# Optimization experiments

Measured on AMD Instinct MI355X. Metric: run time of the kernel, lower is better.

The kernel has to match this reference:

```python
import jax, jax.numpy as jnp
from jax import lax
import numpy as np

G, K = 8, 9  # deformable groups, 3x3 kernel taps


def conv1x1_bn_relu(x, W, scale, bias):
    # Conv2d 1x1 (no bias) + folded eval-mode BatchNorm (per-channel scale/bias) + ReLU
    y = jnp.einsum('bchw,oc->bohw', x, W)
    return jax.nn.relu(y * scale[None, :, None, None] + bias[None, :, None, None])


def dcn_v2(feat, offset_feat, W_om, b_om, W_dcn, b_dcn):
    # Modulated deformable conv v2, 3x3, stride 1, pad 1, dilation 1,
    # deformable_groups=G, extra_offset_mask: offsets/mask predicted from offset_feat.
    B, C, H, W_ = feat.shape
    Cg = C // G
    om = lax.conv_general_dilated(offset_feat, W_om, (1, 1), ((1, 1), (1, 1)))
    om = om + b_om[None, :, None, None]              # [B, 3*G*K, H, W]
    o1, o2, m = jnp.split(om, 3, axis=1)
    off_y = o1.reshape(B, G, K, H, W_)
    off_x = o2.reshape(B, G, K, H, W_)
    mask = jax.nn.sigmoid(m).reshape(B, G, K, H, W_)
    dk = jnp.arange(3) - 1
    dkh = jnp.repeat(dk, 3)   # tap row offset,  k = kh*3 + kw
    dkw = jnp.tile(dk, 3)     # tap col offset
    hh = jnp.arange(H, dtype=feat.dtype)
    ww = jnp.arange(W_, dtype=feat.dtype)
    py = hh[None, None, None, :, None] + dkh[None, None, :, None, None].astype(feat.dtype) + off_y
    px = ww[None, None, None, None, :] + dkw[None, None, :, None, None].astype(feat.dtype) + off_x
    y0 = jnp.floor(py); x0 = jnp.floor(px)
    ty = py - y0; tx = px - x0
    xg = feat.reshape(B, G, Cg, H * W_)

    def gather(idx):  # idx [B,G,K,H,W] int32 -> [B,G,Cg,K,H,W]
        f = lambda xf, i: xf[:, i]
        return jax.vmap(jax.vmap(f))(xg, idx)

    val = jnp.zeros((B, G, Cg, K, H, W_), dtype=feat.dtype)
    y0i = y0.astype(jnp.int32); x0i = x0.astype(jnp.int32)
    for dy, wy in ((0, 1.0 - ty), (1, ty)):
        iy = y0i + dy
        vy = (iy >= 0) & (iy < H)
        iyc = jnp.clip(iy, 0, H - 1)
        for dx, wx in ((0, 1.0 - tx), (1, tx)):
            ix = x0i + dx
            v = vy & (ix >= 0) & (ix < W_)
            idx = iyc * W_ + jnp.clip(ix, 0, W_ - 1)
            w = (wy * wx) * v.astype(feat.dtype)      # zero-padding outside
            val = val + w[:, :, None] * gather(idx)
    val = val * mask[:, :, None]                      # modulation
    Wd = W_dcn.reshape(W_dcn.shape[0], G, Cg, K)      # [Cout, G, Cg, K]
    out = jnp.einsum('bgckhw,ogck->bohw', val, Wd) + b_dcn[None, :, None, None]
    return out


def setup_inputs() -> dict:
    key = jax.random.key(0)
    ks = jax.random.split(key, 16)
    B, C, H, W_ = 8, 128, 64, 64
    Cd = C // 2  # dcn out channels = 64
    d = {}
    d['feat_l'] = jax.random.normal(ks[0], (B, C, H, W_), jnp.float32)
    d['feat_s'] = jax.random.normal(ks[1], (B, C, H // 2, W_ // 2), jnp.float32)
    d['W_fsm'] = jax.random.normal(ks[2], (C, C), jnp.float32) / np.sqrt(C)
    d['s_fsm'] = 1.0 + 0.1 * jax.random.normal(ks[3], (C,), jnp.float32)
    d['b_fsm'] = 0.1 * jax.random.normal(ks[4], (C,), jnp.float32)
    d['W_off'] = jax.random.normal(ks[5], (C, 2 * C), jnp.float32) / np.sqrt(2 * C)
    d['s_off'] = 1.0 + 0.1 * jax.random.normal(ks[6], (C,), jnp.float32)
    d['b_off'] = 0.1 * jax.random.normal(ks[7], (C,), jnp.float32)
    d['W_om'] = 0.05 * jax.random.normal(ks[8], (3 * G * K, C, 3, 3), jnp.float32)
    d['b_om'] = jnp.zeros((3 * G * K,), jnp.float32)
    d['W_dcn'] = jax.random.normal(ks[9], (Cd, C, 3, 3), jnp.float32) / np.sqrt(C * 9)
    d['b_dcn'] = 0.1 * jax.random.normal(ks[10], (Cd,), jnp.float32)
    d['W_cat'] = jax.random.normal(ks[11], (C, Cd), jnp.float32) / np.sqrt(Cd)
    d['s_cat'] = 1.0 + 0.1 * jax.random.normal(ks[12], (C,), jnp.float32)
    d['b_cat'] = 0.1 * jax.random.normal(ks[13], (C,), jnp.float32)
    return d


def reference(feat_l, feat_s, W_fsm, s_fsm, b_fsm, W_off, s_off, b_off,
              W_om, b_om, W_dcn, b_dcn, W_cat, s_cat, b_cat):
    # nearest upsample x2 (F.interpolate nearest to feat_l spatial size)
    feat_up = jnp.repeat(jnp.repeat(feat_s, 2, axis=2), 2, axis=3)
    feat_arm = conv1x1_bn_relu(feat_l, W_fsm, s_fsm, b_fsm)
    offset = conv1x1_bn_relu(jnp.concatenate([feat_arm, feat_up * 2.0], axis=1),
                             W_off, s_off, b_off)
    feat_align = jax.nn.relu(dcn_v2(feat_up, offset, W_om, b_om, W_dcn, b_dcn))
    feat = conv1x1_bn_relu(feat_align, W_cat, s_cat, b_cat) + feat_arm
    return (feat, feat_arm)
```

## Files before the change

### kernel.cpp

```cpp
#include <hip/hip_runtime.h>


typedef __attribute__((ext_vector_type(8))) short short8;
typedef __attribute__((ext_vector_type(4))) float f32x4;
typedef _Float16 __attribute__((ext_vector_type(2))) h2;

static __device__ __forceinline__ unsigned short f2bf(float x) {
    union { float f; unsigned int u; } v; v.f = x;
    return (unsigned short)((v.u + 0x7FFF + ((v.u >> 16) & 1)) >> 16);
}
static __device__ __forceinline__ unsigned short f2h(float x) {
    union { _Float16 h; unsigned short u; } v; v.h = (_Float16)x;
    return v.u;
}

__global__ __launch_bounds__(256) void k_prepfs(const float* __restrict__ fs,
        uint4* __restrict__ fsT4, uint4* __restrict__ fsH4) {
    __shared__ unsigned short st[64 * 136];
    unsigned int* st32 = (unsigned int*)st;
    const int t = threadIdx.x;
    const int b = blockIdx.x >> 4;
    const int p0 = (blockIdx.x & 15) << 6;
    for (int i = t; i < 64 * 64; i += 256) {
        int c2 = i >> 6, px = i & 63;
        float v0 = fs[(((b << 7) + 2 * c2) << 10) + p0 + px];
        float v1 = fs[(((b << 7) + 2 * c2 + 1) << 10) + p0 + px];
        st32[px * 68 + c2] = (unsigned int)f2bf(v0) | ((unsigned int)f2bf(v1) << 16);
    }
    __syncthreads();
    for (int i = t; i < 64 * 16; i += 256) {
        int px = i >> 4, q = i & 15;
        fsT4[(((b << 10) + p0 + px) << 4) + q] = ((const uint4*)(st + px * 136))[q];
    }
    __syncthreads();
    for (int i = t; i < 64 * 64; i += 256) {
        int c2 = i >> 6, px = i & 63;
        float v0 = fs[(((b << 7) + 2 * c2) << 10) + p0 + px];
        float v1 = fs[(((b << 7) + 2 * c2 + 1) << 10) + p0 + px];
        st32[px * 68 + c2] = (unsigned int)f2h(v0) | ((unsigned int)f2h(v1) << 16);
    }
    __syncthreads();
    for (int i = t; i < 64 * 16; i += 256) {
        int px = i >> 4, q = i & 15;
        fsH4[(((b << 10) + p0 + px) << 4) + q] = ((const uint4*)(st + px * 136))[q];
    }
}

__global__ __launch_bounds__(256) void k_packall(
        const float* __restrict__ W_fsm, const float* __restrict__ W_off,
        const float* __restrict__ W_cat, const float* __restrict__ W_dcn,
        const float* __restrict__ W_om,
        unsigned short* __restrict__ wbfsm, unsigned short* __restrict__ wboff,
        unsigned short* __restrict__ wbcat, unsigned short* __restrict__ wbdcn,
        unsigned short* __restrict__ wb2) {
    int idx = blockIdx.x * 256 + threadIdx.x;
    int lane = idx & 63;
    int ml = lane & 15, kl = (lane >> 4) * 8;
    unsigned short tmp[8];
    if (idx < 2048) {
        int r = idx >> 6;
        int o = (r % 8) * 16 + ml, k0 = (r / 8) * 32 + kl;
#pragma unroll
        for (int j = 0; j < 8; j++) tmp[j] = f2bf(W_fsm[o * 128 + k0 + j]);
        ((uint4*)wbfsm)[idx] = *(const uint4*)tmp;
    } else if (idx < 6144) {
        int i2 = idx - 2048;
        int r = i2 >> 6;
        int o = (r % 8) * 16 + ml, k0 = (r / 8) * 32 + kl;
#pragma unroll
        for (int j = 0; j < 8; j++) {
            int k = k0 + j;
            float f = W_off[o * 256 + k];
            if (k >= 128) f *= 2.0f;
            tmp[j] = f2bf(f);
        }
        ((uint4*)wboff)[i2] = *(const uint4*)tmp;
    } else if (idx < 7168) {
        int i2 = idx - 6144;
        int r = i2 >> 6;
        int o = (r % 8) * 16 + ml, k0 = (r / 8) * 32 + kl;
#pragma unroll
        for (int j = 0; j < 8; j++) tmp[j] = f2bf(W_cat[o * 64 + k0 + j]);
        ((uint4*)wbcat)[i2] = *(const uint4*)tmp;
    } else if (idx < 16384) {
        int i2 = idx - 7168;
        int r = i2 >> 6;
        int o = (r & 3) * 16 + ml, k0 = (r >> 2) * 32 + kl;
#pragma unroll
        for (int j = 0; j < 8; j++) {
            int k = k0 + j;
            int g = k / 144;
            int rem = k - g * 144;
            tmp[j] = f2h(W_dcn[(o * 128 + g * 16 + (rem & 15)) * 9 + (rem >> 4)]);
        }
        ((uint4*)wbdcn)[i2] = *(const uint4*)tmp;
    } else if (idx < 53248) {
        int i2 = idx - 16384;
        int r = i2 >> 6;
        int nt = r & 15, kk = r >> 4;
        int tap = kk >> 2, cc = kk & 3;
        int o = nt * 16 + ml;
        int c0 = cc * 32 + kl;
#pragma unroll
        for (int j = 0; j < 8; j++) {
            float v = (o < 216) ? W_om[(o * 128 + (c0 + j)) * 9 + tap] : 0.0f;
            tmp[j] = f2bf(v);
        }
        ((uint4*)wb2)[i2] = *(const uint4*)tmp;
    }
}

__global__ __launch_bounds__(512, 4) void k12(const float* __restrict__ feat_l,
        const uint4* __restrict__ fsT4,
        const unsigned short* __restrict__ wbf, const unsigned short* __restrict__ wbo,
        const float* __restrict__ s_fsm, const float* __restrict__ b_fsm,
        const float* __restrict__ s_off, const float* __restrict__ b_off,
        float* __restrict__ feat_arm, unsigned short* __restrict__ offT) {
    __shared__ unsigned short A1[64 * 136];
    __shared__ unsigned short A2[64 * 264];
    float* E32 = (float*)A1;
    const int t = threadIdx.x;
    const int b = blockIdx.x >> 6;
    const int h = blockIdx.x & 63;
    const int hw0 = h << 6;
    unsigned int* A1w = (unsigned int*)A1;
    for (int i = t; i < 64 * 64; i += 512) {
        int c2 = i >> 6, px = i & 63;
        float v0 = feat_l[(((b << 7) + 2 * c2) << 12) + hw0 + px];
        float v1 = feat_l[(((b << 7) + 2 * c2 + 1) << 12) + hw0 + px];
        A1w[px * 68 + c2] = (unsigned int)f2bf(v0) | ((unsigned int)f2bf(v1) << 16);
    }
    {
        const int h2 = h >> 1;
        int px2 = t >> 4, q = t & 15;
        uint4 v = fsT4[(((b << 10) + (h2 << 5) + px2) << 4) + q];
        ((uint4*)(A2 + (2 * px2) * 264 + 128))[q] = v;
        ((uint4*)(A2 + (2 * px2 + 1) * 264 + 128))[q] = v;
    }
    __syncthreads();
    const int lane = t & 63;
    const int w = __builtin_amdgcn_readfirstlane(t >> 6);
    const int pq = w & 3;
    const int nh = w >> 2;
    const int m = lane & 15, ko = lane >> 4;
    f32x4 acc[4];
#pragma unroll
    for (int nt2 = 0; nt2 < 4; nt2++) acc[nt2] = (f32x4){0.f, 0.f, 0.f, 0.f};
#pragma unroll
    for (int kk = 0; kk < 4; kk++) {
        short8 av = *(const short8*)(A1 + (pq * 16 + m) * 136 + kk * 32 + ko * 8);
        const uint4* wb = (const uint4*)wbf + (kk * 8 + nh * 4) * 64 + lane;
#pragma unroll
        for (int nt2 = 0; nt2 < 4; nt2++) {
            uint4 bu = wb[nt2 * 64];
            acc[nt2] = __builtin_amdgcn_mfma_f32_16x16x32_bf16(av, *(short8*)&bu, acc[nt2], 0, 0, 0);
        }
    }
#pragma unroll
    for (int nt2 = 0; nt2 < 4; nt2++) {
        int o = ((nh << 2) + nt2) * 16 + m;
        float sc = s_fsm[o], bi = b_fsm[o];
#pragma unroll
        for (int r = 0; r < 4; r++) {
            float v = fmaf(acc[nt2][r], sc, bi);
            v = v > 0.f ? v : 0.f;
            acc[nt2][r] = v;
            A2[(pq * 16 + ko * 4 + r) * 264 + o] = f2bf(v);
        }
    }
#pragma unroll 1
    for (int half = 0; half < 2; half++) {
        __syncthreads();
        if (nh == half) {
#pragma unroll
            for (int nt2 = 0; nt2 < 4; nt2++)
#pragma unroll
                for (int r = 0; r < 4; r++)
                    E32[(pq * 16 + ko * 4 + r) * 67 + nt2 * 16 + m] = acc[nt2][r];
        }
        __syncthreads();
        for (int i = t; i < 4096; i += 512) {
            int ol = i >> 6, pp = i & 63;
            feat_arm[(((b << 7) + half * 64 + ol) << 12) + hw0 + pp] = E32[pp * 67 + ol];
        }
    }
    __syncthreads();
    f32x4 acc2[4];
#pragma unroll
    for (int nt2 = 0; nt2 < 4; nt2++) acc2[nt2] = (f32x4){0.f, 0.f, 0.f, 0.f};
#pragma unroll
    for (int kk = 0; kk < 8; kk++) {
        short8 av = *(const short8*)(A2 + (pq * 16 + m) * 264 + kk * 32 + ko * 8);
        const uint4* wb = (const uint4*)wbo + (kk * 8 + nh * 4) * 64 + lane;
#pragma unroll
        for (int nt2 = 0; nt2 < 4; nt2++) {
            uint4 bu = wb[nt2 * 64];
            acc2[nt2] = __builtin_amdgcn_mfma_f32_16x16x32_bf16(av, *(short8*)&bu, acc2[nt2], 0, 0, 0);
        }
    }
    __syncthreads();
#pragma unroll
    for (int nt2 = 0; nt2 < 4; nt2++) {
        int o = ((nh << 2) + nt2) * 16 + m;
        float sc = s_off[o], bi = b_off[o];
#pragma unroll
        for (int r = 0; r < 4; r++) {
            float v = fmaf(acc2[nt2][r], sc, bi);
            v = v > 0.f ? v : 0.f;
            A2[(pq * 16 + ko * 4 + r) * 264 + o] = f2bf(v);
        }
    }
    __syncthreads();
    for (int i = t; i < 64 * 16; i += 512) {
        int px = i >> 4, q = i & 15;
        ((uint4*)offT)[(((b << 12) + hw0 + px) << 4) + q] = ((const uint4*)(A2 + px * 264))[q];
    }
}

__global__ __launch_bounds__(512, 4) void k_omdcn(
        const unsigned short* __restrict__ offT, const uint4* __restrict__ fsH4,
        const unsigned short* __restrict__ Wb2, const float* __restrict__ bom,
        const unsigned short* __restrict__ wbd, const float* __restrict__ bd,
        const unsigned short* __restrict__ wbc,
        const float* __restrict__ s_cat, const float* __restrict__ b_cat,
        const float* __restrict__ feat_arm, float* __restrict__ feat) {
    __shared__ float LDSf[16384];
    unsigned short* st = (unsigned short*)LDSf;
    float* omT = LDSf;
    float* Rbuf = LDSf;
    unsigned short* A3 = (unsigned short*)(LDSf + 13888);
    float* T = LDSf;
    const uint4* offT4 = (const uint4*)offT;
    const uint4* W4 = (const uint4*)Wb2;
    const int t = threadIdx.x;
    const int b = blockIdx.x >> 6;
    const int h = blockIdx.x & 63;
    for (int i = t; i < 3 * 66 * 16; i += 512) {
        int q = i & 15;
        int rp = i >> 4;
        int r = rp / 66, p = rp - r * 66;
        int gy = h + r - 1, gx = p - 1;
        uint4 v = make_uint4(0, 0, 0, 0);
        if (gy >= 0 && gy < 64 && gx >= 0 && gx < 64)
            v = offT4[((((b << 6) + gy) << 6) + gx) * 16 + q];
        ((uint4*)(st + rp * 136))[q] = v;
    }
    __syncthreads();
    const int lane = t & 63;
    const int w = __builtin_amdgcn_readfirstlane(t >> 6);
    const int nq = w & 3;
    const int kh = w >> 2;
    const int m = lane & 15, ko = lane >> 4;
    f32x4 acc[16];
#pragma unroll
    for (int i = 0; i < 16; i++) acc[i] = (f32x4){0.f, 0.f, 0.f, 0.f};
    {
        const int kk0 = kh * 18;
#pragma unroll 4
        for (int kki = 0; kki < 18; kki++) {
            const int kk = kk0 + kki;
            const int tap = kk >> 2, cc = kk & 3;
            const int dy = tap / 3, dx = tap - dy * 3;
            uint4 b4[4];
#pragma unroll
            for (int nt2 = 0; nt2 < 4; nt2++)
                b4[nt2] = W4[(((kk << 4) + (nq << 2) + nt2) << 6) + lane];
            short8 a8[4];
#pragma unroll
            for (int mt = 0; mt < 4; mt++) {
                int p = mt * 16 + m + dx;
                a8[mt] = *(const short8*)(st + (dy * 66 + p) * 136 + (cc << 5) + (ko << 3));
            }
#pragma unroll
            for (int nt2 = 0; nt2 < 4; nt2++)
#pragma unroll
                for (int mt = 0; mt < 4; mt++)
                    acc[nt2 * 4 + mt] = __builtin_amdgcn_mfma_f32_16x16x32_bf16(
                        a8[mt], *(short8*)&b4[nt2], acc[nt2 * 4 + mt], 0, 0, 0);
        }
    }
    __syncthreads();
    if (kh == 0) {
#pragma unroll
        for (int nt2 = 0; nt2 < 4; nt2++) {
            int o = ((nq << 2) + nt2) * 16 + m;
            if (o < 216) {
                float bv = bom[o];
#pragma unroll
                for (int mt = 0; mt < 4; mt++) {
                    f32x4 v = acc[nt2 * 4 + mt];
#pragma unroll
                    for (int r = 0; r < 4; r++)
                        omT[(mt * 16 + (ko << 2) + r) * 217 + o] = v[r] + bv;
                }
            }
        }
    }
    __syncthreads();
    if (kh == 1) {
#pragma unroll
        for (int nt2 = 0; nt2 < 4; nt2++) {
            int o = ((nq << 2) + nt2) * 16 + m;
            if (o < 216) {
#pragma unroll
                for (int mt = 0; mt < 4; mt++) {
                    f32x4 v = acc[nt2 * 4 + mt];
#pragma unroll
                    for (int r = 0; r < 4; r++)
                        omT[(mt * 16 + (ko << 2) + r) * 217 + o] += v[r];
                }
            }
        }
    }
    __syncthreads();
    const int px = (nq << 4) + m;
    const float fh = (float)h, fw = (float)px;
    const int pb_ = b << 10;
    const float* omrow = omT + px * 217;
    f32x4 accd[4];
#pragma unroll
    for (int nt = 0; nt < 4; nt++) accd[nt] = (f32x4){0.f, 0.f, 0.f, 0.f};
    {
        const int dk0 = kh * 18;
#pragma unroll
        for (int kki = 0; kki < 18; kki++) {
            const int kk = dk0 + kki;
            int k0 = (kk << 5) + (ko << 3);
            int g = k0 / 144;
            int rem = k0 - g * 144;
            int tap = rem >> 4;
            int c0 = rem & 15;
            int ch = g * 9 + tap;
            float oy = omrow[ch];
            float ox = omrow[72 + ch];
            float mmv = omrow[144 + ch];
            mmv = 1.0f / (1.0f + __expf(-mmv));
            float py = fh + (float)(tap / 3 - 1) + oy;
            float pxx = fw + (float)(tap % 3 - 1) + ox;
            float y0f = floorf(py), x0f = floorf(pxx);
            float tyf = py - y0f, txf = pxx - x0f;
            int y0i = (int)y0f, x0i = (int)x0f;
            int y1i = y0i + 1, x1i = x0i + 1;
            bool vy0 = (y0i >= 0) && (y0i < 64);
            bool vy1 = (y1i >= 0) && (y1i < 64);
            bool vx0 = (x0i >= 0) && (x0i < 64);
            bool vx1 = (x1i >= 0) && (x1i < 64);
            float w00 = (vy0 && vx0) ? (1.0f - tyf) * (1.0f - txf) * mmv : 0.0f;
            float w01 = (vy0 && vx1) ? (1.0f - tyf) * txf * mmv : 0.0f;
            float w10 = (vy1 && vx0) ? tyf * (1.0f - txf) * mmv : 0.0f;
            float w11 = (vy1 && vx1) ? tyf * txf * mmv : 0.0f;
            int yc0 = y0i < 0 ? 0 : (y0i > 63 ? 63 : y0i);
            int yc1 = y1i < 0 ? 0 : (y1i > 63 ? 63 : y1i);
            int xc0 = x0i < 0 ? 0 : (x0i > 63 ? 63 : x0i);
            int xc1 = x1i < 0 ? 0 : (x1i > 63 ? 63 : x1i);
            int row0 = (yc0 >> 1) << 5, row1 = (yc1 >> 1) << 5;
            int ci = g * 2 + (c0 >> 3);
            union { uint4 u; h2 h[4]; } C00, C01, C10, C11;
            C00.u = fsH4[((pb_ + row0 + (xc0 >> 1)) << 4) + ci];
            C01.u = fsH4[((pb_ + row0 + (xc1 >> 1)) << 4) + ci];
            C10.u = fsH4[((pb_ + row1 + (xc0 >> 1)) << 4) + ci];
            C11.u = fsH4[((pb_ + row1 + (xc1 >> 1)) << 4) + ci];
            _Float16 h00 = (_Float16)w00, h01 = (_Float16)w01;
            _Float16 h10 = (_Float16)w10, h11 = (_Float16)w11;
            h2 W00 = (h2){h00, h00}, W01 = (h2){h01, h01};
            h2 W10 = (h2){h10, h10}, W11 = (h2){h11, h11};
            union { short8 s; h2 h[4]; } av;
#pragma unroll
            for (int c = 0; c < 4; c++)
                av.h[c] = C00.h[c] * W00 + C01.h[c] * W01 + C10.h[c] * W10 + C11.h[c] * W11;
            const uint4* wb = (const uint4*)wbd + (kk << 2) * 64 + lane;
#pragma unroll
            for (int nt = 0; nt < 4; nt++) {
                uint4 bu = wb[nt * 64];
                accd[nt] = __builtin_amdgcn_mfma_f32_16x16x32_f16(av.s, *(short8*)&bu, accd[nt], 0, 0, 0);
            }
        }
    }
    __syncthreads();
    if (kh == 1) {
#pragma unroll
        for (int nt = 0; nt < 4; nt++)
            *(f32x4*)(Rbuf + ((nq << 6) + lane) * 20 + (nt << 2)) = accd[nt];
    }
    __syncthreads();
    if (kh == 0) {
#pragma unroll
        for (int nt = 0; nt < 4; nt++)
            accd[nt] += *(const f32x4*)(Rbuf + ((nq << 6) + lane) * 20 + (nt << 2));
#pragma unroll
        for (int nt = 0; nt < 4; nt++) {
            int o = (nt << 4) + m;
            float bv = bd[o];
#pragma unroll
            for (int r = 0; r < 4; r++) {
                float v = accd[nt][r] + bv;
                v = v > 0.f ? v : 0.f;
                A3[((nq << 4) + (ko << 2) + r) * 72 + o] = f2bf(v);
            }
        }
    }
    __syncthreads();
    f32x4 acc2[4];
#pragma unroll
    for (int nt2 = 0; nt2 < 4; nt2++) acc2[nt2] = (f32x4){0.f, 0.f, 0.f, 0.f};
#pragma unroll
    for (int kk2 = 0; kk2 < 2; kk2++) {
        short8 av = *(const short8*)(A3 + ((nq << 4) + m) * 72 + kk2 * 32 + (ko << 3));
#pragma unroll
        for (int nt2 = 0; nt2 < 4; nt2++) {
            uint4 bu = ((const uint4*)wbc)[(kk2 * 8 + (kh << 2) + nt2) * 64 + lane];
            acc2[nt2] = __builtin_amdgcn_mfma_f32_16x16x32_bf16(av, *(short8*)&bu, acc2[nt2], 0, 0, 0);
        }
    }
#pragma unroll 1
    for (int half = 0; half < 2; half++) {
        __syncthreads();
        if (kh == half) {
#pragma unroll
            for (int nt2 = 0; nt2 < 4; nt2++) {
                int o = (((kh << 2) + nt2) << 4) + m;
                float sc = s_cat[o], bi = b_cat[o];
#pragma unroll
                for (int r = 0; r < 4; r++) {
                    float v = fmaf(acc2[nt2][r], sc, bi);
                    v = v > 0.f ? v : 0.f;
                    T[((nq << 4) + (ko << 2) + r) * 67 + (nt2 << 4) + m] = v;
                }
            }
        }
        __syncthreads();
        for (int i = t; i < 4096; i += 512) {
            int ol = i >> 6, pp = i & 63;
            int gidx = (((b << 7) + half * 64 + ol) << 12) + (h << 6) + pp;
            feat[gidx] = T[pp * 67 + ol] + feat_arm[gidx];
        }
    }
}

extern "C" void kernel_launch(void* const* d_in, const int* in_sizes, int n_in,
                              void* d_out, int out_size, void* d_ws, size_t ws_size,
                              hipStream_t stream) {
    const float* feat_l = (const float*)d_in[0];
    const float* feat_s = (const float*)d_in[1];
    const float* W_fsm  = (const float*)d_in[2];
    const float* s_fsm  = (const float*)d_in[3];
    const float* b_fsm  = (const float*)d_in[4];
    const float* W_off  = (const float*)d_in[5];
    const float* s_off  = (const float*)d_in[6];
    const float* b_off  = (const float*)d_in[7];
    const float* W_om   = (const float*)d_in[8];
    const float* b_om   = (const float*)d_in[9];
    const float* W_dcn  = (const float*)d_in[10];
    const float* b_dcn  = (const float*)d_in[11];
    const float* W_cat  = (const float*)d_in[12];
    const float* s_cat  = (const float*)d_in[13];
    const float* b_cat  = (const float*)d_in[14];

    float* feat     = (float*)d_out;
    float* feat_arm = feat + 4194304;

    float* ws = (float*)d_ws;
    unsigned short* offT = (unsigned short*)ws;
    uint4* fsT4  = (uint4*)(ws + 9175040);
    unsigned short* wb2   = (unsigned short*)(ws + 9699328);
    unsigned short* wbfsm = (unsigned short*)(ws + 9846784);
    unsigned short* wboff = (unsigned short*)(ws + 9854976);
    unsigned short* wbcat = (unsigned short*)(ws + 9871360);
    unsigned short* wbdcn = (unsigned short*)(ws + 9875456);
    uint4* fsH4  = (uint4*)(ws + 9912320);

    k_prepfs<<<128, 256, 0, stream>>>(feat_s, fsT4, fsH4);
    k_packall<<<208, 256, 0, stream>>>(W_fsm, W_off, W_cat, W_dcn, W_om,
                                       wbfsm, wboff, wbcat, wbdcn, wb2);

    k12<<<512, 512, 0, stream>>>(feat_l, fsT4, wbfsm, wboff,
                                 s_fsm, b_fsm, s_off, b_off, feat_arm, offT);
    k_omdcn<<<512, 512, 0, stream>>>(offT, fsH4, wb2, b_om, wbdcn, b_dcn,
                                     wbcat, s_cat, b_cat, feat_arm, feat);
}
```

Measured before the change: 176.2 us.

## Merge prep kernels, channel-major fp16 feature layout, prefetch weights, pair DCN gathers

Merges the feature-conversion and weight-packing kernels into one launch to cut a kernel launch. Stores the fp16 upsample-source features channel-group-major, so lanes gathering the same channel chunk touch neighbouring pixels. Software-prefetches the next offset-conv weight fragment in registers, and splits the DCN loop into prep/consume halves processed in pairs so two taps' gathers are in flight before their MFMAs. This raises register pressure under launch bounds of 512 threads with 4 blocks, which may cause spills.

```diff
diff --git a/kernel.cpp b/kernel.cpp
--- a/kernel.cpp
+++ b/kernel.cpp
@@ -14,46 +14,46 @@
     return v.u;
 }
 
-__global__ __launch_bounds__(256) void k_prepfs(const float* __restrict__ fs,
-        uint4* __restrict__ fsT4, uint4* __restrict__ fsH4) {
-    __shared__ unsigned short st[64 * 136];
-    unsigned int* st32 = (unsigned int*)st;
-    const int t = threadIdx.x;
-    const int b = blockIdx.x >> 4;
-    const int p0 = (blockIdx.x & 15) << 6;
-    for (int i = t; i < 64 * 64; i += 256) {
-        int c2 = i >> 6, px = i & 63;
-        float v0 = fs[(((b << 7) + 2 * c2) << 10) + p0 + px];
-        float v1 = fs[(((b << 7) + 2 * c2 + 1) << 10) + p0 + px];
-        st32[px * 68 + c2] = (unsigned int)f2bf(v0) | ((unsigned int)f2bf(v1) << 16);
-    }
-    __syncthreads();
-    for (int i = t; i < 64 * 16; i += 256) {
-        int px = i >> 4, q = i & 15;
-        fsT4[(((b << 10) + p0 + px) << 4) + q] = ((const uint4*)(st + px * 136))[q];
-    }
-    __syncthreads();
-    for (int i = t; i < 64 * 64; i += 256) {
-        int c2 = i >> 6, px = i & 63;
-        float v0 = fs[(((b << 7) + 2 * c2) << 10) + p0 + px];
-        float v1 = fs[(((b << 7) + 2 * c2 + 1) << 10) + p0 + px];
-        st32[px * 68 + c2] = (unsigned int)f2h(v0) | ((unsigned int)f2h(v1) << 16);
-    }
-    __syncthreads();
-    for (int i = t; i < 64 * 16; i += 256) {
-        int px = i >> 4, q = i & 15;
-        fsH4[(((b << 10) + p0 + px) << 4) + q] = ((const uint4*)(st + px * 136))[q];
-    }
-}
-
-__global__ __launch_bounds__(256) void k_packall(
+__global__ __launch_bounds__(256) void k_prep(const float* __restrict__ fs,
+        uint4* __restrict__ fsT4, uint4* __restrict__ fsC4,
         const float* __restrict__ W_fsm, const float* __restrict__ W_off,
         const float* __restrict__ W_cat, const float* __restrict__ W_dcn,
         const float* __restrict__ W_om,
         unsigned short* __restrict__ wbfsm, unsigned short* __restrict__ wboff,
         unsigned short* __restrict__ wbcat, unsigned short* __restrict__ wbdcn,
         unsigned short* __restrict__ wb2) {
-    int idx = blockIdx.x * 256 + threadIdx.x;
+    __shared__ unsigned short st[64 * 136];
+    const int t = threadIdx.x;
+    if (blockIdx.x < 128) {
+        unsigned int* st32 = (unsigned int*)st;
+        const int b = blockIdx.x >> 4;
+        const int p0 = (blockIdx.x & 15) << 6;
+        for (int i = t; i < 64 * 64; i += 256) {
+            int c2 = i >> 6, px = i & 63;
+            float v0 = fs[(((b << 7) + 2 * c2) << 10) + p0 + px];
+            float v1 = fs[(((b << 7) + 2 * c2 + 1) << 10) + p0 + px];
+            st32[px * 68 + c2] = (unsigned int)f2bf(v0) | ((unsigned int)f2bf(v1) << 16);
+        }
+        __syncthreads();
+        for (int i = t; i < 64 * 16; i += 256) {
+            int px = i >> 4, q = i & 15;
+            fsT4[(((b << 10) + p0 + px) << 4) + q] = ((const uint4*)(st + px * 136))[q];
+        }
+        __syncthreads();
+        for (int i = t; i < 64 * 64; i += 256) {
+            int c2 = i >> 6, px = i & 63;
+            float v0 = fs[(((b << 7) + 2 * c2) << 10) + p0 + px];
+            float v1 = fs[(((b << 7) + 2 * c2 + 1) << 10) + p0 + px];
+            st32[px * 68 + c2] = (unsigned int)f2h(v0) | ((unsigned int)f2h(v1) << 16);
+        }
+        __syncthreads();
+        for (int i = t; i < 64 * 16; i += 256) {
+            int ci = i >> 6, px = i & 63;
+            fsC4[(b << 14) + (ci << 10) + p0 + px] = ((const uint4*)(st + px * 136))[ci];
+        }
+        return;
+    }
+    int idx = (blockIdx.x - 128) * 256 + t;
     int lane = idx & 63;
     int ml = lane & 15, kl = (lane >> 4) * 8;
     unsigned short tmp[8];
@@ -217,8 +217,71 @@
     }
 }
 
+static __device__ __forceinline__ void dcn_prep(int kk, int ko, const float* omrow,
+        float fh, float fw, const uint4* __restrict__ fsC4, int b14,
+        uint4& c00, uint4& c01, uint4& c10, uint4& c11,
+        float& w00, float& w01, float& w10, float& w11) {
+    int k0 = (kk << 5) + (ko << 3);
+    int g = k0 / 144;
+    int rem = k0 - g * 144;
+    int tap = rem >> 4;
+    int c0 = rem & 15;
+    int ch = g * 9 + tap;
+    float oy = omrow[ch];
+    float ox = omrow[72 + ch];
+    float mmv = omrow[144 + ch];
+    mmv = 1.0f / (1.0f + __expf(-mmv));
+    float py = fh + (float)(tap / 3 - 1) + oy;
+    float pxx = fw + (float)(tap % 3 - 1) + ox;
+    float y0f = floorf(py), x0f = floorf(pxx);
+    float tyf = py - y0f, txf = pxx - x0f;
+    int y0i = (int)y0f, x0i = (int)x0f;
+    int y1i = y0i + 1, x1i = x0i + 1;
+    bool vy0 = (y0i >= 0) && (y0i < 64);
+    bool vy1 = (y1i >= 0) && (y1i < 64);
+    bool vx0 = (x0i >= 0) && (x0i < 64);
+    bool vx1 = (x1i >= 0) && (x1i < 64);
+    w00 = (vy0 && vx0) ? (1.0f - tyf) * (1.0f - txf) * mmv : 0.0f;
+    w01 = (vy0 && vx1) ? (1.0f - tyf) * txf * mmv : 0.0f;
+    w10 = (vy1 && vx0) ? tyf * (1.0f - txf) * mmv : 0.0f;
+    w11 = (vy1 && vx1) ? tyf * txf * mmv : 0.0f;
+    int yc0 = y0i < 0 ? 0 : (y0i > 63 ? 63 : y0i);
+    int yc1 = y1i < 0 ? 0 : (y1i > 63 ? 63 : y1i);
+    int xc0 = x0i < 0 ? 0 : (x0i > 63 ? 63 : x0i);
+    int xc1 = x1i < 0 ? 0 : (x1i > 63 ? 63 : x1i);
+    int row0 = (yc0 >> 1) << 5, row1 = (yc1 >> 1) << 5;
+    int ci = g * 2 + (c0 >> 3);
+    const uint4* base = fsC4 + b14 + (ci << 10);
+    c00 = base[row0 + (xc0 >> 1)];
+    c01 = base[row0 + (xc1 >> 1)];
+    c10 = base[row1 + (xc0 >> 1)];
+    c11 = base[row1 + (xc1 >> 1)];
+}
+
+static __device__ __forceinline__ void dcn_consume(int kk,
+        const uint4& c00, const uint4& c01, const uint4& c10, const uint4& c11,
+        float w00, float w01, float w10, float w11,
+        const uint4* __restrict__ wbd4, int lane, f32x4* accd) {
+    _Float16 h00 = (_Float16)w00, h01 = (_Float16)w01;
+    _Float16 h10 = (_Float16)w10, h11 = (_Float16)w11;
+    h2 W00 = (h2){h00, h00}, W01 = (h2){h01, h01};
+    h2 W10 = (h2){h10, h10}, W11 = (h2){h11, h11};
+    union { uint4 u; h2 h[4]; } U00, U01, U10, U11;
+    U00.u = c00; U01.u = c01; U10.u = c10; U11.u = c11;
+    union { short8 s; h2 h[4]; } av;
+#pragma unroll
+    for (int c = 0; c < 4; c++)
+        av.h[c] = U00.h[c] * W00 + U01.h[c] * W01 + U10.h[c] * W10 + U11.h[c] * W11;
+    const uint4* wb = wbd4 + (kk << 2) * 64 + lane;
+#pragma unroll
+    for (int nt = 0; nt < 4; nt++) {
+        uint4 bu = wb[nt * 64];
+        accd[nt] = __builtin_amdgcn_mfma_f32_16x16x32_f16(av.s, *(short8*)&bu, accd[nt], 0, 0, 0);
+    }
+}
+
 __global__ __launch_bounds__(512, 4) void k_omdcn(
-        const unsigned short* __restrict__ offT, const uint4* __restrict__ fsH4,
+        const unsigned short* __restrict__ offT, const uint4* __restrict__ fsC4,
         const unsigned short* __restrict__ Wb2, const float* __restrict__ bom,
         const unsigned short* __restrict__ wbd, const float* __restrict__ bd,
         const unsigned short* __restrict__ wbc,
@@ -232,6 +295,7 @@
     float* T = LDSf;
     const uint4* offT4 = (const uint4*)offT;
     const uint4* W4 = (const uint4*)Wb2;
+    const uint4* wbd4 = (const uint4*)wbd;
     const int t = threadIdx.x;
     const int b = blockIdx.x >> 6;
     const int h = blockIdx.x & 63;
@@ -256,15 +320,21 @@
     for (int i = 0; i < 16; i++) acc[i] = (f32x4){0.f, 0.f, 0.f, 0.f};
     {
         const int kk0 = kh * 18;
-#pragma unroll 4
+        uint4 b4[4];
+#pragma unroll
+        for (int nt2 = 0; nt2 < 4; nt2++)
+            b4[nt2] = W4[(((kk0 << 4) + (nq << 2) + nt2) << 6) + lane];
+#pragma unroll
         for (int kki = 0; kki < 18; kki++) {
             const int kk = kk0 + kki;
             const int tap = kk >> 2, cc = kk & 3;
             const int dy = tap / 3, dx = tap - dy * 3;
-            uint4 b4[4];
-#pragma unroll
-            for (int nt2 = 0; nt2 < 4; nt2++)
-                b4[nt2] = W4[(((kk << 4) + (nq << 2) + nt2) << 6) + lane];
+            uint4 b4n[4];
+            if (kki < 17) {
+#pragma unroll
+                for (int nt2 = 0; nt2 < 4; nt2++)
+                    b4n[nt2] = W4[((((kk + 1) << 4) + (nq << 2) + nt2) << 6) + lane];
+            }
             short8 a8[4];
 #pragma unroll
             for (int mt = 0; mt < 4; mt++) {
@@ -277,6 +347,10 @@
                 for (int mt = 0; mt < 4; mt++)
                     acc[nt2 * 4 + mt] = __builtin_amdgcn_mfma_f32_16x16x32_bf16(
                         a8[mt], *(short8*)&b4[nt2], acc[nt2 * 4 + mt], 0, 0, 0);
+            if (kki < 17) {
+#pragma unroll
+                for (int nt2 = 0; nt2 < 4; nt2++) b4[nt2] = b4n[nt2];
+            }
         }
     }
     __syncthreads();
@@ -315,7 +389,7 @@
     __syncthreads();
     const int px = (nq << 4) + m;
     const float fh = (float)h, fw = (float)px;
-    const int pb_ = b << 10;
+    const int b14 = b << 14;
     const float* omrow = omT + px * 217;
     f32x4 accd[4];
 #pragma unroll
@@ -323,57 +397,17 @@
     {
         const int dk0 = kh * 18;
 #pragma unroll
-        for (int kki = 0; kki < 18; kki++) {
-            const int kk = dk0 + kki;
-            int k0 = (kk << 5) + (ko << 3);
-            int g = k0 / 144;
-            int rem = k0 - g * 144;
-            int tap = rem >> 4;
-            int c0 = rem & 15;
-            int ch = g * 9 + tap;
-            float oy = omrow[ch];
-            float ox = omrow[72 + ch];
-            float mmv = omrow[144 + ch];
-            mmv = 1.0f / (1.0f + __expf(-mmv));
-            float py = fh + (float)(tap / 3 - 1) + oy;
-            float pxx = fw + (float)(tap % 3 - 1) + ox;
-            float y0f = floorf(py), x0f = floorf(pxx);
-            float tyf = py - y0f, txf = pxx - x0f;
-            int y0i = (int)y0f, x0i = (int)x0f;
-            int y1i = y0i + 1, x1i = x0i + 1;
-            bool vy0 = (y0i >= 0) && (y0i < 64);
-            bool vy1 = (y1i >= 0) && (y1i < 64);
-            bool vx0 = (x0i >= 0) && (x0i < 64);
-            bool vx1 = (x1i >= 0) && (x1i < 64);
-            float w00 = (vy0 && vx0) ? (1.0f - tyf) * (1.0f - txf) * mmv : 0.0f;
-            float w01 = (vy0 && vx1) ? (1.0f - tyf) * txf * mmv : 0.0f;
-            float w10 = (vy1 && vx0) ? tyf * (1.0f - txf) * mmv : 0.0f;
-            float w11 = (vy1 && vx1) ? tyf * txf * mmv : 0.0f;
-            int yc0 = y0i < 0 ? 0 : (y0i > 63 ? 63 : y0i);
-            int yc1 = y1i < 0 ? 0 : (y1i > 63 ? 63 : y1i);
-            int xc0 = x0i < 0 ? 0 : (x0i > 63 ? 63 : x0i);
-            int xc1 = x1i < 0 ? 0 : (x1i > 63 ? 63 : x1i);
-            int row0 = (yc0 >> 1) << 5, row1 = (yc1 >> 1) << 5;
-            int ci = g * 2 + (c0 >> 3);
-            union { uint4 u; h2 h[4]; } C00, C01, C10, C11;
-            C00.u = fsH4[((pb_ + row0 + (xc0 >> 1)) << 4) + ci];
-            C01.u = fsH4[((pb_ + row0 + (xc1 >> 1)) << 4) + ci];
-            C10.u = fsH4[((pb_ + row1 + (xc0 >> 1)) << 4) + ci];
-            C11.u = fsH4[((pb_ + row1 + (xc1 >> 1)) << 4) + ci];
-            _Float16 h00 = (_Float16)w00, h01 = (_Float16)w01;
-            _Float16 h10 = (_Float16)w10, h11 = (_Float16)w11;
-            h2 W00 = (h2){h00, h00}, W01 = (h2){h01, h01};
-            h2 W10 = (h2){h10, h10}, W11 = (h2){h11, h11};
-            union { short8 s; h2 h[4]; } av;
-#pragma unroll
-            for (int c = 0; c < 4; c++)
-                av.h[c] = C00.h[c] * W00 + C01.h[c] * W01 + C10.h[c] * W10 + C11.h[c] * W11;
-            const uint4* wb = (const uint4*)wbd + (kk << 2) * 64 + lane;
-#pragma unroll
-            for (int nt = 0; nt < 4; nt++) {
-                uint4 bu = wb[nt * 64];
-                accd[nt] = __builtin_amdgcn_mfma_f32_16x16x32_f16(av.s, *(short8*)&bu, accd[nt], 0, 0, 0);
-            }
+        for (int kp = 0; kp < 9; kp++) {
+            const int kkA = dk0 + 2 * kp;
+            const int kkB = kkA + 1;
+            uint4 a00, a01, a10, a11, e00, e01, e10, e11;
+            float wa00, wa01, wa10, wa11, wb00, wb01, wb10, wb11;
+            dcn_prep(kkA, ko, omrow, fh, fw, fsC4, b14,
+                     a00, a01, a10, a11, wa00, wa01, wa10, wa11);
+            dcn_prep(kkB, ko, omrow, fh, fw, fsC4, b14,
+                     e00, e01, e10, e11, wb00, wb01, wb10, wb11);
+            dcn_consume(kkA, a00, a01, a10, a11, wa00, wa01, wa10, wa11, wbd4, lane, accd);
+            dcn_consume(kkB, e00, e01, e10, e11, wb00, wb01, wb10, wb11, wbd4, lane, accd);
         }
     }
     __syncthreads();
@@ -467,14 +501,13 @@
     unsigned short* wboff = (unsigned short*)(ws + 9854976);
     unsigned short* wbcat = (unsigned short*)(ws + 9871360);
     unsigned short* wbdcn = (unsigned short*)(ws + 9875456);
-    uint4* fsH4  = (uint4*)(ws + 9912320);
-
-    k_prepfs<<<128, 256, 0, stream>>>(feat_s, fsT4, fsH4);
-    k_packall<<<208, 256, 0, stream>>>(W_fsm, W_off, W_cat, W_dcn, W_om,
-                                       wbfsm, wboff, wbcat, wbdcn, wb2);
+    uint4* fsC4  = (uint4*)(ws + 9912320);
+
+    k_prep<<<336, 256, 0, stream>>>(feat_s, fsT4, fsC4, W_fsm, W_off, W_cat,
+                                    W_dcn, W_om, wbfsm, wboff, wbcat, wbdcn, wb2);
 
     k12<<<512, 512, 0, stream>>>(feat_l, fsT4, wbfsm, wboff,
                                  s_fsm, b_fsm, s_off, b_off, feat_arm, offT);
-    k_omdcn<<<512, 512, 0, stream>>>(offT, fsH4, wb2, b_om, wbdcn, b_dcn,
+    k_omdcn<<<512, 512, 0, stream>>>(offT, fsC4, wb2, b_om, wbdcn, b_dcn,
                                      wbcat, s_cat, b_cat, feat_arm, feat);
 }
```

Measured after the change: 161.7 us. 8.3% less time.
